# Optimization experiments

Hardware: AMD Instinct MI355X
Metric: run time of the kernel (lower is better)

Reference implementation:

```python
import jax, jax.numpy as jnp
import numpy as np

EMBED_DIM = 1024
NUM_HEADS = 16
HEAD_DIM = EMBED_DIM // NUM_HEADS
B, S = 4, 2048


def setup_inputs() -> dict:
    key = jax.random.key(0)
    ks = jax.random.split(key, 9)
    sc = 1.0 / np.sqrt(EMBED_DIM)
    d = {"x": jax.random.normal(ks[0], (B, S, EMBED_DIM), jnp.float32)}
    for i, name in enumerate(["q", "k", "v", "out"]):
        d[f"w_{name}"] = jax.random.uniform(ks[1 + 2 * i], (EMBED_DIM, EMBED_DIM), jnp.float32, -sc, sc)
        d[f"b_{name}"] = jax.random.uniform(ks[2 + 2 * i], (EMBED_DIM,), jnp.float32, -sc, sc)
    return d


def reference(x, w_q, b_q, w_k, b_k, w_v, b_v, w_out, b_out):
    b, s, e = x.shape
    # projections (PyTorch Linear: x @ W.T + b)
    q = (x @ w_q.T + b_q).reshape(b, s, NUM_HEADS, HEAD_DIM).transpose(0, 2, 1, 3)
    k = (x @ w_k.T + b_k).reshape(b, s, NUM_HEADS, HEAD_DIM).transpose(0, 2, 1, 3)
    v = (x @ w_v.T + b_v).reshape(b, s, NUM_HEADS, HEAD_DIM).transpose(0, 2, 1, 3)
    scores = jnp.einsum("bhqd,bhkd->bhqk", q, k) / np.sqrt(HEAD_DIM).astype(np.float32)
    attn = jax.nn.softmax(scores, axis=-1)  # dropout p=0.0 -> identity
    out = jnp.einsum("bhqk,bhkd->bhqd", attn, v)
    out = out.transpose(0, 2, 1, 3).reshape(b, s, e)
    return out @ w_out.T + b_out
```

## Files before the change

kernel.cpp:

```cpp
#include <hip/hip_runtime.h>


typedef __bf16 bf16x8 __attribute__((ext_vector_type(8)));
typedef __bf16 bf16x2 __attribute__((ext_vector_type(2)));
typedef __bf16 bf16x4v __attribute__((ext_vector_type(4)));
typedef float  f32x4  __attribute__((ext_vector_type(4)));
typedef unsigned short u16x4 __attribute__((ext_vector_type(4)));

#define BB 4
#define SS 2048
#define EE 1024
#define HH 16
#define DD 64
#define MM 8192
#define GK 1024
#define GN 1024

static __device__ __forceinline__ unsigned short f2bf(float f) {
  unsigned int u = __float_as_uint(f);
  u += 0x7fffu + ((u >> 16) & 1u);
  return (unsigned short)(u >> 16);
}

static __device__ __forceinline__ void gld_lds16(const void* g, void* l) {
  __builtin_amdgcn_global_load_lds((__attribute__((address_space(1))) void*)g,
                                   (__attribute__((address_space(3))) void*)l,
                                   16, 0, 0);
}

__global__ __launch_bounds__(256) void cvt_all(
    const float* __restrict__ x,  const float* __restrict__ wq,
    const float* __restrict__ wk, const float* __restrict__ wv,
    const float* __restrict__ wo,
    unsigned short* __restrict__ xb,  unsigned short* __restrict__ wqb,
    unsigned short* __restrict__ wkb, unsigned short* __restrict__ wvb,
    unsigned short* __restrict__ wob) {
  const unsigned long long NX = 8ull * 1024 * 1024;
  const unsigned long long NW = 1024ull * 1024;
  unsigned long long i = (unsigned long long)blockIdx.x * 256 + threadIdx.x;
  unsigned long long e = i * 4;
  const float* src; unsigned short* dst; unsigned long long off;
  if (e < NX) { src = x; dst = xb; off = e; }
  else {
    unsigned long long j = e - NX;
    unsigned int wi = (unsigned int)(j >> 20);
    off = j & (NW - 1);
    src = (wi == 0) ? wq : (wi == 1) ? wk : (wi == 2) ? wv : wo;
    dst = (wi == 0) ? wqb : (wi == 1) ? wkb : (wi == 2) ? wvb : wob;
  }
  float4 v = *(const float4*)(src + off);
  u16x4 o; o.x = f2bf(v.x); o.y = f2bf(v.y); o.z = f2bf(v.z); o.w = f2bf(v.w);
  *(u16x4*)(dst + off) = o;
}

template <int MODE>
__global__ __launch_bounds__(256, 2) void gemm2(
    const unsigned short* __restrict__ A,
    const unsigned short* __restrict__ B0, const unsigned short* __restrict__ B1,
    const float* __restrict__ bias0, const float* __restrict__ bias1,
    void* __restrict__ out0, void* __restrict__ out1) {
  __shared__ __align__(16) unsigned short As[128 * 64];
  __shared__ __align__(16) unsigned short Bs[128 * 64];
  const int tid = threadIdx.x, lane = tid & 63, w = tid >> 6;
  const int l15 = lane & 15, quad = lane >> 4;
  const int wm = w & 1, wn = w >> 1;
  const int m0 = blockIdx.y * 128;

  const unsigned short* Bt; const float* bias; void* out; float osc; int n0w;
  if (MODE == 0) {
    int sel = (blockIdx.x >= 8);
    Bt = sel ? B1 : B0; bias = sel ? bias1 : bias0; out = sel ? out1 : out0;
    osc = sel ? 1.0f : 0.125f;
    n0w = (blockIdx.x & 7) * 128;
  } else {
    Bt = B0; bias = bias0; out = out0; osc = 1.0f;
    n0w = blockIdx.x * 128;
  }

  f32x4 acc[4][4] = {};

  for (int k0 = 0; k0 < GK; k0 += 64) {
    __syncthreads();
#pragma unroll
    for (int t = 0; t < 4; ++t) {
      int cb = (w * 4 + t) * 64;
      int c = cb + lane, r = c >> 3, g = ((c & 7) + r) & 7;
      gld_lds16(A + (size_t)(m0 + r) * GK + k0 + g * 8, &As[cb * 8]);
    }
#pragma unroll
    for (int t = 0; t < 4; ++t) {
      int cb = (w * 4 + t) * 64;
      int c = cb + lane, r = c >> 3, g = ((c & 7) + r) & 7;
      gld_lds16(Bt + (size_t)(n0w + r) * GK + k0 + g * 8, &Bs[cb * 8]);
    }
    __builtin_amdgcn_s_waitcnt(0);
    __syncthreads();
#pragma unroll
    for (int ks = 0; ks < 2; ++ks) {
      const int s = (ks * 4 + quad - l15) & 7;
      bf16x8 af[4], bfr[4];
#pragma unroll
      for (int mi = 0; mi < 4; ++mi)
        af[mi] = *(const bf16x8*)&As[(wm * 64 + mi * 16 + l15) * 64 + s * 8];
#pragma unroll
      for (int ni = 0; ni < 4; ++ni)
        bfr[ni] = *(const bf16x8*)&Bs[(wn * 64 + ni * 16 + l15) * 64 + s * 8];
#pragma unroll
      for (int mi = 0; mi < 4; ++mi)
#pragma unroll
        for (int ni = 0; ni < 4; ++ni) {
          if (MODE == 1)
            acc[mi][ni] = __builtin_amdgcn_mfma_f32_16x16x32_bf16(
                af[mi], bfr[ni], acc[mi][ni], 0, 0, 0);
          else
            acc[ni][mi] = __builtin_amdgcn_mfma_f32_16x16x32_bf16(
                bfr[ni], af[mi], acc[ni][mi], 0, 0, 0);
        }
    }
  }
  if (MODE == 1) {
#pragma unroll
    for (int ni = 0; ni < 4; ++ni) {
      int n = n0w + wn * 64 + ni * 16 + l15;
      float bv = bias[n];
      int h = n >> 6, d = n & 63;
#pragma unroll
      for (int mi = 0; mi < 4; ++mi) {
        int mb = m0 + wm * 64 + mi * 16 + quad * 4;
        int b = mb >> 11, s = mb & 2047;
        bf16x4v o;
#pragma unroll
        for (int r = 0; r < 4; ++r) o[r] = (__bf16)(acc[mi][ni][r] + bv);
        *(bf16x4v*)&((unsigned short*)out)[((size_t)(b * HH + h) * DD + d) * SS + s] = o;
      }
    }
  } else {
#pragma unroll
    for (int ni = 0; ni < 4; ++ni) {
      int nb = n0w + wn * 64 + ni * 16 + quad * 4;
      float4 b4 = *(const float4*)&bias[nb];
#pragma unroll
      for (int mi = 0; mi < 4; ++mi) {
        int m = m0 + wm * 64 + mi * 16 + l15;
        if (MODE == 0) {
          int b = m >> 11, s = m & 2047, h = nb >> 6, d = nb & 63;
          bf16x4v o;
          o[0] = (__bf16)((acc[ni][mi][0] + b4.x) * osc);
          o[1] = (__bf16)((acc[ni][mi][1] + b4.y) * osc);
          o[2] = (__bf16)((acc[ni][mi][2] + b4.z) * osc);
          o[3] = (__bf16)((acc[ni][mi][3] + b4.w) * osc);
          *(bf16x4v*)&((unsigned short*)out)[((size_t)(b * HH + h) * SS + s) * DD + d] = o;
        } else {
          float4 st;
          st.x = acc[ni][mi][0] + b4.x; st.y = acc[ni][mi][1] + b4.y;
          st.z = acc[ni][mi][2] + b4.z; st.w = acc[ni][mi][3] + b4.w;
          *(float4*)&((float*)out)[(size_t)m * GN + nb] = st;
        }
      }
    }
  }
}

__global__ __launch_bounds__(256, 3) void attn(
    const unsigned short* __restrict__ Q,
    const unsigned short* __restrict__ K,
    const unsigned short* __restrict__ Vt,
    unsigned short* __restrict__ O) {
  __shared__ __align__(16) unsigned short Ks[2][64 * 64];
  __shared__ __align__(16) unsigned short Vs[2][64 * 64];
  const int tid = threadIdx.x, lane = tid & 63, w = tid >> 6;
  const int l15 = lane & 15, quad = lane >> 4;
  const int bh = blockIdx.x >> 4;
  const int q0 = (blockIdx.x & 15) * 128;
  const int b = bh >> 4, h = bh & 15;

  const unsigned short* Qb = Q + (size_t)bh * SS * DD;
  const unsigned short* Kb = K + (size_t)bh * SS * DD;
  const unsigned short* Vb = Vt + (size_t)bh * DD * SS;

  bf16x8 qf[2][2];
#pragma unroll
  for (int qb = 0; qb < 2; ++qb) {
    int qrow = q0 + w * 32 + qb * 16 + l15;
    qf[qb][0] = *(const bf16x8*)&Qb[(size_t)qrow * DD + quad * 8];
    qf[qb][1] = *(const bf16x8*)&Qb[(size_t)qrow * DD + 32 + quad * 8];
  }

  f32x4 oaccT[4][2] = {};
  float lrow[2] = {0.f, 0.f};
  const int qodd = quad & 1;
  const int Rcore = (l15 >> 2) * 8 + (l15 & 3);
  const int Rpar = ((l15 >> 2) & 1) * 4;

#pragma unroll
  for (int t = 0; t < 2; ++t) {
    int cb = (w * 2 + t) * 64;
    int c = cb + lane, r = c >> 3, g = ((c & 7) + r) & 7;
    gld_lds16(Kb + (size_t)r * DD + g * 8, &Ks[0][cb * 8]);
    gld_lds16(Vb + (size_t)r * SS + g * 8, &Vs[0][cb * 8]);
  }
  __syncthreads();

  for (int kt = 0; kt < SS / 64; ++kt) {
    const int cur = kt & 1;
    if (kt + 1 < SS / 64) {
      const int k0n = (kt + 1) * 64, nxt = cur ^ 1;
#pragma unroll
      for (int t = 0; t < 2; ++t) {
        int cb = (w * 2 + t) * 64;
        int c = cb + lane, r = c >> 3, g = ((c & 7) + r) & 7;
        gld_lds16(Kb + (size_t)(k0n + r) * DD + g * 8, &Ks[nxt][cb * 8]);
        gld_lds16(Vb + (size_t)r * SS + k0n + g * 8, &Vs[nxt][cb * 8]);
      }
    }
    const unsigned short* Kc = Ks[cur];
    const unsigned short* Vc = Vs[cur];

    int pk[2][2][2][2];
#pragma unroll
    for (int ks = 0; ks < 2; ++ks)
#pragma unroll
      for (int beta = 0; beta < 2; ++beta) {
        const int R = ks * 32 + Rcore + (beta ? (4 - Rpar) : Rpar);
        const int s0 = (quad - R) & 7, s1 = (4 + quad - R) & 7;
        const bf16x8 kf0 = *(const bf16x8*)&Kc[R * 64 + s0 * 8];
        const bf16x8 kf1 = *(const bf16x8*)&Kc[R * 64 + s1 * 8];
#pragma unroll
        for (int qb = 0; qb < 2; ++qb) {
          f32x4 z = {};
          z = __builtin_amdgcn_mfma_f32_16x16x32_bf16(kf0, qf[qb][0], z, 0, 0, 0);
          z = __builtin_amdgcn_mfma_f32_16x16x32_bf16(kf1, qf[qb][1], z, 0, 0, 0);
          float p0 = __expf(z[0]), p1 = __expf(z[1]);
          float p2 = __expf(z[2]), p3 = __expf(z[3]);
          lrow[qb] += (p0 + p1) + (p2 + p3);
          union { bf16x2 h2; int i; } ua, ub;
          ua.h2.x = (__bf16)p0; ua.h2.y = (__bf16)p1;
          ub.h2.x = (__bf16)p2; ub.h2.y = (__bf16)p3;
          pk[qb][ks][beta][0] = ua.i; pk[qb][ks][beta][1] = ub.i;
        }
      }
    union PB { int i[4]; bf16x8 v; } pf[2][2];
#pragma unroll
    for (int qb = 0; qb < 2; ++qb)
#pragma unroll
      for (int ks = 0; ks < 2; ++ks) {
        pf[qb][ks].i[0] = qodd ? pk[qb][ks][1][0] : pk[qb][ks][0][0];
        pf[qb][ks].i[1] = qodd ? pk[qb][ks][1][1] : pk[qb][ks][0][1];
        pf[qb][ks].i[2] = qodd ? pk[qb][ks][0][0] : pk[qb][ks][1][0];
        pf[qb][ks].i[3] = qodd ? pk[qb][ks][0][1] : pk[qb][ks][1][1];
      }
#pragma unroll
    for (int mb = 0; mb < 4; ++mb) {
      const int s0 = (quad - l15) & 7, s1 = (4 + quad - l15) & 7;
      const bf16x8 vf0 = *(const bf16x8*)&Vc[(mb * 16 + l15) * 64 + s0 * 8];
      const bf16x8 vf1 = *(const bf16x8*)&Vc[(mb * 16 + l15) * 64 + s1 * 8];
#pragma unroll
      for (int qb = 0; qb < 2; ++qb) {
        oaccT[mb][qb] = __builtin_amdgcn_mfma_f32_16x16x32_bf16(
            vf0, pf[qb][0].v, oaccT[mb][qb], 0, 0, 0);
        oaccT[mb][qb] = __builtin_amdgcn_mfma_f32_16x16x32_bf16(
            vf1, pf[qb][1].v, oaccT[mb][qb], 0, 0, 0);
      }
    }
    __syncthreads();
  }
#pragma unroll
  for (int qb = 0; qb < 2; ++qb) {
    float l = lrow[qb];
    l += __shfl_xor(l, 16);
    l += __shfl_xor(l, 32);
    float inv = 1.0f / l;
    int q = q0 + w * 32 + qb * 16 + l15;
#pragma unroll
    for (int mb = 0; mb < 4; ++mb) {
      bf16x4v o;
#pragma unroll
      for (int r = 0; r < 4; ++r) o[r] = (__bf16)(oaccT[mb][qb][r] * inv);
      *(bf16x4v*)&O[((size_t)b * SS + q) * EE + h * 64 + mb * 16 + quad * 4] = o;
    }
  }
}

extern "C" void kernel_launch(void* const* d_in, const int* in_sizes, int n_in,
                              void* d_out, int out_size, void* d_ws, size_t ws_size,
                              hipStream_t stream) {
  const float* x  = (const float*)d_in[0];
  const float* wq = (const float*)d_in[1];
  const float* bq = (const float*)d_in[2];
  const float* wk = (const float*)d_in[3];
  const float* bk = (const float*)d_in[4];
  const float* wv = (const float*)d_in[5];
  const float* bv = (const float*)d_in[6];
  const float* wo = (const float*)d_in[7];
  const float* bo = (const float*)d_in[8];

  unsigned short* ws = (unsigned short*)d_ws;
  const size_t MEG = 1024ull * 1024;
  unsigned short* xb  = ws;
  unsigned short* wqb = ws + 8 * MEG;
  unsigned short* wkb = ws + 9 * MEG;
  unsigned short* wvb = ws + 10 * MEG;
  unsigned short* wob = ws + 11 * MEG;
  unsigned short* qb  = ws + 12 * MEG;
  unsigned short* kb  = ws + 20 * MEG;
  unsigned short* vtb = ws + 28 * MEG;
  unsigned short* ob  = xb;

  cvt_all<<<12288, 256, 0, stream>>>(x, wq, wk, wv, wo, xb, wqb, wkb, wvb, wob);
  gemm2<0><<<dim3(16, 64), 256, 0, stream>>>(xb, wqb, wkb, bq, bk, qb, kb);
  gemm2<1><<<dim3(8, 64), 256, 0, stream>>>(xb, wvb, nullptr, bv, nullptr, vtb, nullptr);
  attn<<<BB * HH * (SS / 128), 256, 0, stream>>>(qb, kb, vtb, ob);
  gemm2<2><<<dim3(8, 64), 256, 0, stream>>>(ob, wob, nullptr, bo, nullptr, d_out, nullptr);
}
```

Before: 282.5 us.

## Merge QKV GEMMs into one launch, add XCD-aware block swizzle, use exp2

Merges the Q/K and V projection GEMMs into a single 1536-block launch and splits the output projection into its own kernel. Block indices are remapped in the GEMMs and in attention so that blocks sharing A rows or the same head land on the same XCD, aiming for better L2 reuse. The softmax exponent switches to a native exp2 with log2(e) folded into the Q scale, which trims a multiply per element. K/V prefetch addresses in attention are now advanced by pointer increments rather than recomputed each tile. The single QKV kernel adds a runtime branch on isv around the MFMA loop and epilogue.

```diff
diff --git a/kernel.cpp b/kernel.cpp
--- a/kernel.cpp
+++ b/kernel.cpp
@@ -15,6 +15,13 @@
 #define MM 8192
 #define GK 1024
 #define GN 1024
+#define QSCALE 0.1803368801111354f
+
+#if __has_builtin(__builtin_amdgcn_exp2f)
+#define EXP2(x) __builtin_amdgcn_exp2f(x)
+#else
+#define EXP2(x) __expf(0.6931471805599453f * (x))
+#endif
 
 static __device__ __forceinline__ unsigned short f2bf(float f) {
   unsigned int u = __float_as_uint(f);
@@ -53,29 +60,30 @@
   *(u16x4*)(dst + off) = o;
 }
 
-template <int MODE>
-__global__ __launch_bounds__(256, 2) void gemm2(
+__global__ __launch_bounds__(256, 2) void gemm_qkv(
     const unsigned short* __restrict__ A,
-    const unsigned short* __restrict__ B0, const unsigned short* __restrict__ B1,
-    const float* __restrict__ bias0, const float* __restrict__ bias1,
-    void* __restrict__ out0, void* __restrict__ out1) {
+    const unsigned short* __restrict__ Wq, const unsigned short* __restrict__ Wk,
+    const unsigned short* __restrict__ Wv,
+    const float* __restrict__ Bq, const float* __restrict__ Bk,
+    const float* __restrict__ Bv,
+    unsigned short* __restrict__ Oq, unsigned short* __restrict__ Ok,
+    unsigned short* __restrict__ Ov) {
   __shared__ __align__(16) unsigned short As[128 * 64];
   __shared__ __align__(16) unsigned short Bs[128 * 64];
   const int tid = threadIdx.x, lane = tid & 63, w = tid >> 6;
   const int l15 = lane & 15, quad = lane >> 4;
   const int wm = w & 1, wn = w >> 1;
-  const int m0 = blockIdx.y * 128;
-
-  const unsigned short* Bt; const float* bias; void* out; float osc; int n0w;
-  if (MODE == 0) {
-    int sel = (blockIdx.x >= 8);
-    Bt = sel ? B1 : B0; bias = sel ? bias1 : bias0; out = sel ? out1 : out0;
-    osc = sel ? 1.0f : 0.125f;
-    n0w = (blockIdx.x & 7) * 128;
-  } else {
-    Bt = B0; bias = bias0; out = out0; osc = 1.0f;
-    n0w = blockIdx.x * 128;
-  }
+  const int id = blockIdx.x;
+  const int xcd = id & 7, sid = id >> 3;
+  const int xt = sid >> 3;
+  const int m0 = (xcd * 8 + (sid & 7)) * 128;
+  const int sel = xt >> 3;
+  const int n0w = (xt & 7) * 128;
+  const bool isv = (sel == 2);
+  const unsigned short* Bt = (sel == 0) ? Wq : (sel == 1) ? Wk : Wv;
+  const float* bias = (sel == 0) ? Bq : (sel == 1) ? Bk : Bv;
+  unsigned short* out = (sel == 0) ? Oq : (sel == 1) ? Ok : Ov;
+  const float osc = (sel == 0) ? QSCALE : 1.0f;
 
   f32x4 acc[4][4] = {};
 
@@ -105,20 +113,24 @@
 #pragma unroll
       for (int ni = 0; ni < 4; ++ni)
         bfr[ni] = *(const bf16x8*)&Bs[(wn * 64 + ni * 16 + l15) * 64 + s * 8];
-#pragma unroll
-      for (int mi = 0; mi < 4; ++mi)
-#pragma unroll
-        for (int ni = 0; ni < 4; ++ni) {
-          if (MODE == 1)
+      if (isv) {
+#pragma unroll
+        for (int mi = 0; mi < 4; ++mi)
+#pragma unroll
+          for (int ni = 0; ni < 4; ++ni)
             acc[mi][ni] = __builtin_amdgcn_mfma_f32_16x16x32_bf16(
                 af[mi], bfr[ni], acc[mi][ni], 0, 0, 0);
-          else
+      } else {
+#pragma unroll
+        for (int mi = 0; mi < 4; ++mi)
+#pragma unroll
+          for (int ni = 0; ni < 4; ++ni)
             acc[ni][mi] = __builtin_amdgcn_mfma_f32_16x16x32_bf16(
                 bfr[ni], af[mi], acc[ni][mi], 0, 0, 0);
-        }
-    }
-  }
-  if (MODE == 1) {
+      }
+    }
+  }
+  if (isv) {
 #pragma unroll
     for (int ni = 0; ni < 4; ++ni) {
       int n = n0w + wn * 64 + ni * 16 + l15;
@@ -131,7 +143,7 @@
         bf16x4v o;
 #pragma unroll
         for (int r = 0; r < 4; ++r) o[r] = (__bf16)(acc[mi][ni][r] + bv);
-        *(bf16x4v*)&((unsigned short*)out)[((size_t)(b * HH + h) * DD + d) * SS + s] = o;
+        *(bf16x4v*)&out[((size_t)(b * HH + h) * DD + d) * SS + s] = o;
       }
     }
   } else {
@@ -142,21 +154,78 @@
 #pragma unroll
       for (int mi = 0; mi < 4; ++mi) {
         int m = m0 + wm * 64 + mi * 16 + l15;
-        if (MODE == 0) {
-          int b = m >> 11, s = m & 2047, h = nb >> 6, d = nb & 63;
-          bf16x4v o;
-          o[0] = (__bf16)((acc[ni][mi][0] + b4.x) * osc);
-          o[1] = (__bf16)((acc[ni][mi][1] + b4.y) * osc);
-          o[2] = (__bf16)((acc[ni][mi][2] + b4.z) * osc);
-          o[3] = (__bf16)((acc[ni][mi][3] + b4.w) * osc);
-          *(bf16x4v*)&((unsigned short*)out)[((size_t)(b * HH + h) * SS + s) * DD + d] = o;
-        } else {
-          float4 st;
-          st.x = acc[ni][mi][0] + b4.x; st.y = acc[ni][mi][1] + b4.y;
-          st.z = acc[ni][mi][2] + b4.z; st.w = acc[ni][mi][3] + b4.w;
-          *(float4*)&((float*)out)[(size_t)m * GN + nb] = st;
-        }
-      }
+        int b = m >> 11, s = m & 2047, h = nb >> 6, d = nb & 63;
+        bf16x4v o;
+        o[0] = (__bf16)((acc[ni][mi][0] + b4.x) * osc);
+        o[1] = (__bf16)((acc[ni][mi][1] + b4.y) * osc);
+        o[2] = (__bf16)((acc[ni][mi][2] + b4.z) * osc);
+        o[3] = (__bf16)((acc[ni][mi][3] + b4.w) * osc);
+        *(bf16x4v*)&out[((size_t)(b * HH + h) * SS + s) * DD + d] = o;
+      }
+    }
+  }
+}
+
+__global__ __launch_bounds__(256, 2) void gemm_out(
+    const unsigned short* __restrict__ A, const unsigned short* __restrict__ Bt,
+    const float* __restrict__ bias, float* __restrict__ out) {
+  __shared__ __align__(16) unsigned short As[128 * 64];
+  __shared__ __align__(16) unsigned short Bs[128 * 64];
+  const int tid = threadIdx.x, lane = tid & 63, w = tid >> 6;
+  const int l15 = lane & 15, quad = lane >> 4;
+  const int wm = w & 1, wn = w >> 1;
+  const int id = blockIdx.x;
+  const int sid = id >> 3;
+  const int m0 = ((id & 7) * 8 + (sid & 7)) * 128;
+  const int n0w = (sid >> 3) * 128;
+
+  f32x4 acc[4][4] = {};
+
+  for (int k0 = 0; k0 < GK; k0 += 64) {
+    __syncthreads();
+#pragma unroll
+    for (int t = 0; t < 4; ++t) {
+      int cb = (w * 4 + t) * 64;
+      int c = cb + lane, r = c >> 3, g = ((c & 7) + r) & 7;
+      gld_lds16(A + (size_t)(m0 + r) * GK + k0 + g * 8, &As[cb * 8]);
+    }
+#pragma unroll
+    for (int t = 0; t < 4; ++t) {
+      int cb = (w * 4 + t) * 64;
+      int c = cb + lane, r = c >> 3, g = ((c & 7) + r) & 7;
+      gld_lds16(Bt + (size_t)(n0w + r) * GK + k0 + g * 8, &Bs[cb * 8]);
+    }
+    __builtin_amdgcn_s_waitcnt(0);
+    __syncthreads();
+#pragma unroll
+    for (int ks = 0; ks < 2; ++ks) {
+      const int s = (ks * 4 + quad - l15) & 7;
+      bf16x8 af[4], bfr[4];
+#pragma unroll
+      for (int mi = 0; mi < 4; ++mi)
+        af[mi] = *(const bf16x8*)&As[(wm * 64 + mi * 16 + l15) * 64 + s * 8];
+#pragma unroll
+      for (int ni = 0; ni < 4; ++ni)
+        bfr[ni] = *(const bf16x8*)&Bs[(wn * 64 + ni * 16 + l15) * 64 + s * 8];
+#pragma unroll
+      for (int mi = 0; mi < 4; ++mi)
+#pragma unroll
+        for (int ni = 0; ni < 4; ++ni)
+          acc[ni][mi] = __builtin_amdgcn_mfma_f32_16x16x32_bf16(
+              bfr[ni], af[mi], acc[ni][mi], 0, 0, 0);
+    }
+  }
+#pragma unroll
+  for (int ni = 0; ni < 4; ++ni) {
+    int nb = n0w + wn * 64 + ni * 16 + quad * 4;
+    float4 b4 = *(const float4*)&bias[nb];
+#pragma unroll
+    for (int mi = 0; mi < 4; ++mi) {
+      int m = m0 + wm * 64 + mi * 16 + l15;
+      float4 st;
+      st.x = acc[ni][mi][0] + b4.x; st.y = acc[ni][mi][1] + b4.y;
+      st.z = acc[ni][mi][2] + b4.z; st.w = acc[ni][mi][3] + b4.w;
+      *(float4*)&out[(size_t)m * GN + nb] = st;
     }
   }
 }
@@ -170,8 +239,10 @@
   __shared__ __align__(16) unsigned short Vs[2][64 * 64];
   const int tid = threadIdx.x, lane = tid & 63, w = tid >> 6;
   const int l15 = lane & 15, quad = lane >> 4;
-  const int bh = blockIdx.x >> 4;
-  const int q0 = (blockIdx.x & 15) * 128;
+  const int id = blockIdx.x;
+  const int slot = id >> 3;
+  const int bh = (slot >> 4) * 8 + (id & 7);
+  const int q0 = (slot & 15) * 128;
   const int b = bh >> 4, h = bh & 15;
 
   const unsigned short* Qb = Q + (size_t)bh * SS * DD;
@@ -192,25 +263,30 @@
   const int Rcore = (l15 >> 2) * 8 + (l15 & 3);
   const int Rpar = ((l15 >> 2) & 1) * 4;
 
+  const unsigned short* kp[2];
+  const unsigned short* vp[2];
 #pragma unroll
   for (int t = 0; t < 2; ++t) {
     int cb = (w * 2 + t) * 64;
     int c = cb + lane, r = c >> 3, g = ((c & 7) + r) & 7;
     gld_lds16(Kb + (size_t)r * DD + g * 8, &Ks[0][cb * 8]);
     gld_lds16(Vb + (size_t)r * SS + g * 8, &Vs[0][cb * 8]);
+    kp[t] = Kb + (size_t)(64 + r) * DD + g * 8;
+    vp[t] = Vb + (size_t)r * SS + 64 + g * 8;
   }
   __syncthreads();
 
   for (int kt = 0; kt < SS / 64; ++kt) {
     const int cur = kt & 1;
     if (kt + 1 < SS / 64) {
-      const int k0n = (kt + 1) * 64, nxt = cur ^ 1;
+      const int nxt = cur ^ 1;
 #pragma unroll
       for (int t = 0; t < 2; ++t) {
         int cb = (w * 2 + t) * 64;
-        int c = cb + lane, r = c >> 3, g = ((c & 7) + r) & 7;
-        gld_lds16(Kb + (size_t)(k0n + r) * DD + g * 8, &Ks[nxt][cb * 8]);
-        gld_lds16(Vb + (size_t)r * SS + k0n + g * 8, &Vs[nxt][cb * 8]);
+        gld_lds16(kp[t], &Ks[nxt][cb * 8]);
+        gld_lds16(vp[t], &Vs[nxt][cb * 8]);
+        kp[t] += 64 * DD;
+        vp[t] += 64;
       }
     }
     const unsigned short* Kc = Ks[cur];
@@ -230,8 +306,8 @@
           f32x4 z = {};
           z = __builtin_amdgcn_mfma_f32_16x16x32_bf16(kf0, qf[qb][0], z, 0, 0, 0);
           z = __builtin_amdgcn_mfma_f32_16x16x32_bf16(kf1, qf[qb][1], z, 0, 0, 0);
-          float p0 = __expf(z[0]), p1 = __expf(z[1]);
-          float p2 = __expf(z[2]), p3 = __expf(z[3]);
+          float p0 = EXP2(z[0]), p1 = EXP2(z[1]);
+          float p2 = EXP2(z[2]), p3 = EXP2(z[3]);
           lrow[qb] += (p0 + p1) + (p2 + p3);
           union { bf16x2 h2; int i; } ua, ub;
           ua.h2.x = (__bf16)p0; ua.h2.y = (__bf16)p1;
@@ -307,8 +383,7 @@
   unsigned short* ob  = xb;
 
   cvt_all<<<12288, 256, 0, stream>>>(x, wq, wk, wv, wo, xb, wqb, wkb, wvb, wob);
-  gemm2<0><<<dim3(16, 64), 256, 0, stream>>>(xb, wqb, wkb, bq, bk, qb, kb);
-  gemm2<1><<<dim3(8, 64), 256, 0, stream>>>(xb, wvb, nullptr, bv, nullptr, vtb, nullptr);
+  gemm_qkv<<<1536, 256, 0, stream>>>(xb, wqb, wkb, wvb, bq, bk, bv, qb, kb, vtb);
   attn<<<BB * HH * (SS / 128), 256, 0, stream>>>(qb, kb, vtb, ob);
-  gemm2<2><<<dim3(8, 64), 256, 0, stream>>>(ob, wob, nullptr, bo, nullptr, d_out, nullptr);
-}
+  gemm_out<<<512, 256, 0, stream>>>(ob, wob, bo, (float*)d_out);
+}
```

New measurement: 267.4 us. -5.4%, faster.
